# Kernel optimization log

Measured on AMD Instinct MI355X. Metric: run time of the kernel, lower is better.

Reference implementation:

```python
import jax, jax.numpy as jnp
import numpy as np

B, N, C, H = 16, 512, 384, 6
HD = C // H  # 64
FF = 1152


def _ln(x, w, b, eps=1e-5):
    mu = jnp.mean(x, axis=-1, keepdims=True)
    var = jnp.mean((x - mu) ** 2, axis=-1, keepdims=True)
    return (x - mu) * jax.lax.rsqrt(var + eps) * w + b


def setup_inputs() -> dict:
    key = jax.random.key(0)
    ks = jax.random.split(key, 16)
    rn = lambda k, s, sc=0.02: jax.random.normal(k, s, jnp.float32) * sc
    scale = jnp.float32(HD ** -0.5)
    return {
        "src": jax.random.normal(ks[0], (B, N, C), jnp.float32),
        "pre_w": jnp.ones((C,), jnp.float32), "pre_b": jnp.zeros((C,), jnp.float32),
        "qkv_w": rn(ks[1], (3 * C, C)), "qkv_b": jnp.zeros((3 * C,), jnp.float32),
        "scale": scale, "riem_scale": scale, "grassman_scale": scale,
        "conv_w": rn(ks[2], (H, 3 * H), 0.1), "conv_b": jnp.zeros((H,), jnp.float32),
        "proj_w": rn(ks[3], (C, C)), "proj_b": jnp.zeros((C,), jnp.float32),
        "norm1_w": jnp.ones((C,), jnp.float32), "norm1_b": jnp.zeros((C,), jnp.float32),
        "lin1_w": rn(ks[4], (FF, C)), "lin1_b": jnp.zeros((FF,), jnp.float32),
        "lin2_w": rn(ks[5], (C, FF)), "lin2_b": jnp.zeros((C,), jnp.float32),
    }


def reference(src, pre_w, pre_b, qkv_w, qkv_b, scale, riem_scale, grassman_scale,
              conv_w, conv_b, proj_w, proj_b, norm1_w, norm1_b,
              lin1_w, lin1_b, lin2_w, lin2_b):
    x = _ln(src, pre_w, pre_b)
    qkv = (x @ qkv_w.T + qkv_b).reshape(B, N, 3, H, HD)
    qkv = jnp.transpose(qkv, (2, 0, 3, 1, 4))  # [3,B,H,N,HD]
    q, k, v = qkv[0], qkv[1], qkv[2]

    # Grassmann term: orthonormalize tokens-per-head via reduced QR (N>=HD)
    qgr, _ = jnp.linalg.qr(q)  # [B,H,N,HD]
    kgr, _ = jnp.linalg.qr(k)
    dots = jnp.einsum('bhnd,bhmd->bhnm', qgr, kgr)
    # norm over singleton dim then square == elementwise square
    attn_grass = dots ** 2 * grassman_scale

    # Euclidean dot-product term
    qk = jnp.einsum('bhnd,bhmd->bhnm', q, k)
    attn_eucl = qk * scale

    # Riemannian term: pairwise Frobenius norm between rank-1 covariances
    # ||q_i q_i^T - k_j k_j^T||_F = sqrt(||q_i||^4 + ||k_j||^4 - 2 (q_i.k_j)^2)
    qn2 = jnp.sum(q ** 2, axis=-1)  # [B,H,N]
    kn2 = jnp.sum(k ** 2, axis=-1)
    d2 = qn2[..., :, None] ** 2 + kn2[..., None, :] ** 2 - 2.0 * qk ** 2
    attn_riem = jnp.sqrt(jnp.maximum(d2, 0.0)) * riem_scale

    cat = jnp.concatenate([attn_eucl, attn_riem, attn_grass], axis=1)  # [B,3H,N,N]
    mixed = jnp.einsum('bcnm,oc->bonm', cat, conv_w) + conv_b[None, :, None, None]
    attn_ = jax.nn.softmax(mixed, axis=-1)  # [B,H,N,N]

    out = jnp.einsum('bhnm,bhmd->bhnd', attn_, v)
    out = jnp.transpose(out, (0, 2, 1, 3)).reshape(B, N, C)
    out = out @ proj_w.T + proj_b

    src = src + out
    src = _ln(src, norm1_w, norm1_b)
    h = jax.nn.gelu(src @ lin1_w.T + lin1_b, approximate=False)
    src2 = h @ lin2_w.T + lin2_b
    src = src + src2
    return src, attn_
```

## Files before the change

kernel.cpp:

```cpp
#include <hip/hip_runtime.h>
#include <cstdint>
#include <cstddef>

#define DEVI static __device__ __forceinline__

typedef __bf16 bf16x8 __attribute__((ext_vector_type(8)));
typedef float f32x4 __attribute__((ext_vector_type(4)));
typedef unsigned short u16;
typedef unsigned int u32;

DEVI float b2f(u16 h){ u32 x = ((u32)h) << 16; float f; __builtin_memcpy(&f, &x, 4); return f; }
DEVI u16 f2b(float f){ u32 x; __builtin_memcpy(&x, &f, 4); u32 r = (x + 0x7FFFu + ((x >> 16) & 1u)) >> 16; return (u16)r; }

union V16 { uint4 u; bf16x8 v; u16 h[8]; };

DEVI bf16x8 ld16(const u16* p){ V16 t; t.u = *(const uint4*)p; return t.v; }
DEVI f32x4 fzero(){ f32x4 z; z[0]=0.f; z[1]=0.f; z[2]=0.f; z[3]=0.f; return z; }
DEVI f32x4 mm(bf16x8 a, bf16x8 b, f32x4 c){ return __builtin_amdgcn_mfma_f32_16x16x32_bf16(a, b, c, 0, 0, 0); }
DEVI uint4 cvt8(const float* p){
  float4 a = *(const float4*)p, b = *(const float4*)(p + 4);
  V16 t; t.h[0]=f2b(a.x); t.h[1]=f2b(a.y); t.h[2]=f2b(a.z); t.h[3]=f2b(a.w);
  t.h[4]=f2b(b.x); t.h[5]=f2b(b.y); t.h[6]=f2b(b.z); t.h[7]=f2b(b.w); return t.u;
}

__global__ __launch_bounds__(256) void k_ln_src(const float* __restrict__ in, const float* __restrict__ w,
                                                const float* __restrict__ bias, u16* __restrict__ out){
  int wave = threadIdx.x >> 6, lane = threadIdx.x & 63;
  int row = blockIdx.x * 4 + wave;
  const float* p = in + (size_t)row * 384;
  float v[6], s = 0.f, sq = 0.f;
  for(int i = 0; i < 6; i++){ v[i] = p[lane + 64*i]; s += v[i]; sq += v[i]*v[i]; }
  for(int off = 1; off < 64; off <<= 1){ s += __shfl_xor(s, off); sq += __shfl_xor(sq, off); }
  float mu = s * (1.f/384.f), var = sq * (1.f/384.f) - mu*mu;
  float rstd = rsqrtf(fmaxf(var, 0.f) + 1e-5f);
  for(int i = 0; i < 6; i++){
    int j = lane + 64*i;
    out[(size_t)row*384 + j] = f2b((v[i]-mu)*rstd*w[j] + bias[j]);
  }
}

__global__ __launch_bounds__(256) void k_ln_mid(const float* __restrict__ in, const float* __restrict__ w,
                                                const float* __restrict__ bias, u16* __restrict__ outb,
                                                float* __restrict__ outf){
  int wave = threadIdx.x >> 6, lane = threadIdx.x & 63;
  int row = blockIdx.x * 4 + wave;
  const float* p = in + (size_t)row * 384;
  float v[6], s = 0.f, sq = 0.f;
  for(int i = 0; i < 6; i++){ v[i] = p[lane + 64*i]; s += v[i]; sq += v[i]*v[i]; }
  for(int off = 1; off < 64; off <<= 1){ s += __shfl_xor(s, off); sq += __shfl_xor(sq, off); }
  float mu = s * (1.f/384.f), var = sq * (1.f/384.f) - mu*mu;
  float rstd = rsqrtf(fmaxf(var, 0.f) + 1e-5f);
  for(int i = 0; i < 6; i++){
    int j = lane + 64*i;
    float o = (v[i]-mu)*rstd*w[j] + bias[j];
    outb[(size_t)row*384 + j] = f2b(o);
    outf[(size_t)row*384 + j] = o;
  }
}

template<int MODE, int KDIM, int NOUT>
__global__ __launch_bounds__(256,2) void k_gemm(
    const u16* __restrict__ A, const float* __restrict__ W, const float* __restrict__ bias,
    u16* __restrict__ o0, u16* __restrict__ o1, u16* __restrict__ o2,
    const float* __restrict__ res, float* __restrict__ fout)
{
  __shared__ __align__(16) u16 As[128][72];
  __shared__ __align__(16) u16 Bs[128][72];
  const int tid = threadIdx.x, wv = tid >> 6, lane = tid & 63, quad = lane >> 4, l15 = lane & 15;
  constexpr int NB = NOUT / 128;
  const int m0 = (blockIdx.x / NB) * 128, n0 = (blockIdx.x % NB) * 128;
  const int wr = (wv >> 1) * 64, wc = (wv & 1) * 64;
  f32x4 acc[4][4];
  for(int i = 0; i < 4; i++) for(int j = 0; j < 4; j++) acc[i][j] = fzero();
  for(int kt = 0; kt < KDIM; kt += 64){
    for(int i = 0; i < 4; i++){
      int c = tid + i*256; int row = c >> 3, col = (c & 7) * 8;
      *(uint4*)&As[row][col] = *(const uint4*)&A[(size_t)(m0+row)*KDIM + kt + col];
      *(uint4*)&Bs[row][col] = cvt8(&W[(size_t)(n0+row)*KDIM + kt + col]);
    }
    __syncthreads();
    for(int hf = 0; hf < 2; hf++){
      bf16x8 af[4], bf_[4];
      for(int t = 0; t < 4; t++) af[t]  = ld16(&As[wr + t*16 + l15][hf*32 + quad*8]);
      for(int t = 0; t < 4; t++) bf_[t] = ld16(&Bs[wc + t*16 + l15][hf*32 + quad*8]);
      for(int mt = 0; mt < 4; mt++) for(int nt = 0; nt < 4; nt++)
        acc[mt][nt] = mm(af[mt], bf_[nt], acc[mt][nt]);
    }
    __syncthreads();
  }
  for(int mt = 0; mt < 4; mt++) for(int nt = 0; nt < 4; nt++){
    const int gcol = n0 + wc + nt*16 + l15;
    const float bv = bias[gcol];
    for(int r = 0; r < 4; r++){
      const int grow = m0 + wr + mt*16 + quad*4 + r;
      float val = acc[mt][nt][r] + bv;
      if constexpr(MODE == 0){
        int s = gcol / 384, rem = gcol - s*384, h = rem >> 6, d = rem & 63;
        int bb = grow >> 9, n = grow & 511;
        u16* t = (s == 0) ? o0 : ((s == 1) ? o1 : o2);
        t[(((size_t)(bb*6 + h))*512 + n)*64 + d] = f2b(val);
      } else if constexpr(MODE == 1){
        val += res[(size_t)grow*384 + gcol];
        fout[(size_t)grow*384 + gcol] = val;
      } else {
        float g = 0.5f * val * (1.f + erff(val * 0.70710678118654752f));
        o0[(size_t)grow*1152 + gcol] = f2b(g);
      }
    }
  }
}

__global__ __launch_bounds__(256,1) void k_cholqr(
    const u16* __restrict__ qb, const u16* __restrict__ kb,
    u16* __restrict__ aqb, u16* __restrict__ akb,
    float* __restrict__ qn4, float* __restrict__ kn4)
{
  __shared__ float G[64][65];
  __shared__ float invd[64];
  const int tid = threadIdx.x, wv = tid >> 6, lane = tid & 63, quad = lane >> 4, l15 = lane & 15;
  const int blk = blockIdx.x;
  const int isk = blk >= 96; const int bh = isk ? blk - 96 : blk;
  const u16* M = (isk ? kb : qb) + (size_t)bh * 512 * 64;
  u16* Ao = (isk ? akb : aqb) + (size_t)bh * 512 * 64;
  float* n4 = (isk ? kn4 : qn4) + bh * 512;
  for(int rr = tid; rr < 512; rr += 256){
    const u16* p = M + (size_t)rr * 64;
    float s = 0.f;
    for(int i = 0; i < 8; i++){ V16 c; c.u = *(const uint4*)&p[i*8];
      for(int j = 0; j < 8; j++){ float x = b2f(c.h[j]); s += x*x; } }
    n4[rr] = s * s;
  }
  f32x4 g4[4];
  for(int jt = 0; jt < 4; jt++) g4[jt] = fzero();
  for(int k0 = 0; k0 < 512; k0 += 32){
    const u16* base = M + (size_t)(k0 + quad*8) * 64;
    V16 a;
    for(int j = 0; j < 8; j++) a.h[j] = base[(size_t)j*64 + wv*16 + l15];
    for(int jt = 0; jt < 4; jt++){
      V16 bb;
      for(int j = 0; j < 8; j++) bb.h[j] = base[(size_t)j*64 + jt*16 + l15];
      g4[jt] = mm(a.v, bb.v, g4[jt]);
    }
  }
  for(int jt = 0; jt < 4; jt++)
    for(int r = 0; r < 4; r++)
      G[wv*16 + quad*4 + r][jt*16 + l15] = g4[jt][r];
  __syncthreads();
  for(int k = 0; k < 64; k++){
    if(tid == 0){ float pv = sqrtf(fmaxf(G[k][k], 1e-12f)); G[k][k] = pv; invd[k] = 1.f / pv; }
    __syncthreads();
    if(tid > k && tid < 64) G[k][tid] *= invd[k];
    __syncthreads();
    float gkl = G[k][lane];
    for(int i = k + 1 + wv; i < 64; i += 4)
      G[i][lane] -= G[k][i] * gkl;
    __syncthreads();
  }
  for(int rr = tid; rr < 512; rr += 256){
    float m[64];
    const u16* p = M + (size_t)rr * 64;
    for(int i = 0; i < 8; i++){ V16 c; c.u = *(const uint4*)&p[i*8];
      for(int j = 0; j < 8; j++) m[i*8 + j] = b2f(c.h[j]); }
    #pragma unroll
    for(int j = 0; j < 64; j++){
      float yj = m[j] * invd[j];
      m[j] = yj;
      #pragma unroll
      for(int i = j + 1; i < 64; i++) m[i] -= yj * G[j][i];
    }
    for(int i = 0; i < 8; i++){ V16 c;
      for(int j = 0; j < 8; j++) c.h[j] = f2b(m[i*8 + j]);
      *(uint4*)&Ao[(size_t)rr*64 + i*8] = c.u; }
  }
}

__global__ __launch_bounds__(256,2) void k_attn(
    const u16* __restrict__ qb, const u16* __restrict__ kb,
    const u16* __restrict__ aqb, const u16* __restrict__ akb,
    const float* __restrict__ qn4, const float* __restrict__ kn4,
    const float* __restrict__ convw, const float* __restrict__ convb,
    const float* __restrict__ scp, const float* __restrict__ rsp, const float* __restrict__ gsp,
    float* __restrict__ attn)
{
  __shared__ __align__(16) u16 qt[6][16][72];
  __shared__ __align__(16) u16 at[6][16][72];
  __shared__ float cw[108];
  __shared__ float cb[6];
  __shared__ float red[6][16][4];
  const int tid = threadIdx.x, wv = tid >> 6, lane = tid & 63, quad = lane >> 4, l15 = lane & 15;
  const int b = blockIdx.x >> 5, n0 = (blockIdx.x & 31) * 16;
  if(tid < 108) cw[tid] = convw[tid];
  if(tid >= 128 && tid < 134) cb[tid - 128] = convb[tid - 128];
  for(int c = tid; c < 768; c += 256){
    int h = c >> 7, rem = c & 127, row = rem >> 3, col = (rem & 7) * 8;
    size_t off = (((size_t)(b*6 + h)) * 512 + (size_t)(n0 + row)) * 64 + col;
    *(uint4*)&qt[h][row][col] = *(const uint4*)&qb[off];
    *(uint4*)&at[h][row][col] = *(const uint4*)&aqb[off];
  }
  __syncthreads();
  const float sc = scp[0], rs = rsp[0], gs = gsp[0];
  float qn4r[6][4];
  for(int h = 0; h < 6; h++)
    for(int r = 0; r < 4; r++)
      qn4r[h][r] = qn4[(b*6 + h)*512 + n0 + quad*4 + r];
  float S[6][4], recS[6][4];
  for(int o = 0; o < 6; o++) for(int r = 0; r < 4; r++) S[o][r] = 0.f;
  for(int phase = 0; phase < 2; phase++){
    for(int mt = 0; mt < 8; mt++){
      const int mcol = wv*128 + mt*16 + l15;
      float L[6][4];
      for(int o = 0; o < 6; o++){ float c0 = cb[o]; for(int r = 0; r < 4; r++) L[o][r] = c0; }
      #pragma unroll
      for(int h = 0; h < 6; h++){
        const size_t krow = (((size_t)(b*6 + h)) * 512 + mcol) * 64 + quad*8;
        bf16x8 kf0 = ld16(kb + krow),  kf1 = ld16(kb + krow + 32);
        bf16x8 af0 = ld16(akb + krow), af1 = ld16(akb + krow + 32);
        bf16x8 qf0 = ld16(&qt[h][l15][quad*8]), qf1 = ld16(&qt[h][l15][32 + quad*8]);
        bf16x8 gf0 = ld16(&at[h][l15][quad*8]), gf1 = ld16(&at[h][l15][32 + quad*8]);
        f32x4 qk = fzero(); qk = mm(qf0, kf0, qk); qk = mm(qf1, kf1, qk);
        f32x4 dd = fzero(); dd = mm(gf0, af0, dd); dd = mm(gf1, af1, dd);
        float kn = kn4[(b*6 + h)*512 + mcol];
        #pragma unroll
        for(int r = 0; r < 4; r++){
          float q_ = qk[r];
          float e  = q_ * sc;
          float d2 = qn4r[h][r] + kn - 2.f * q_ * q_;
          float ri = rs * sqrtf(fmaxf(d2, 0.f));
          float g  = gs * dd[r] * dd[r];
          #pragma unroll
          for(int o = 0; o < 6; o++)
            L[o][r] += cw[o*18 + h]*e + cw[o*18 + 6 + h]*ri + cw[o*18 + 12 + h]*g;
        }
      }
      if(phase == 0){
        for(int o = 0; o < 6; o++) for(int r = 0; r < 4; r++) S[o][r] += __expf(fminf(L[o][r], 80.f));
      } else {
        for(int o = 0; o < 6; o++) for(int r = 0; r < 4; r++){
          float a = __expf(fminf(L[o][r], 80.f)) * recS[o][r];
          attn[(((size_t)(b*6 + o)) * 512 + (n0 + quad*4 + r)) * 512 + mcol] = a;
        }
      }
    }
    if(phase == 0){
      for(int o = 0; o < 6; o++) for(int r = 0; r < 4; r++){
        float s = S[o][r];
        s += __shfl_xor(s, 1); s += __shfl_xor(s, 2); s += __shfl_xor(s, 4); s += __shfl_xor(s, 8);
        if(l15 == 0) red[o][quad*4 + r][wv] = s;
      }
      __syncthreads();
      for(int o = 0; o < 6; o++) for(int r = 0; r < 4; r++){
        int rw = quad*4 + r;
        recS[o][r] = 1.f / (red[o][rw][0] + red[o][rw][1] + red[o][rw][2] + red[o][rw][3]);
      }
      __syncthreads();
    }
  }
}

__global__ __launch_bounds__(256,2) void k_av(const float* __restrict__ attn, const u16* __restrict__ vb,
                                              u16* __restrict__ av)
{
  __shared__ __align__(16) u16 At[128][72];
  __shared__ __align__(16) u16 Vt[64][72];
  const int tid = threadIdx.x, wv = tid >> 6, lane = tid & 63, quad = lane >> 4, l15 = lane & 15;
  const int blk = blockIdx.x, bh = blk >> 2, n0 = (blk & 3) * 128;
  const int b = bh / 6, h = bh - b * 6;
  const float* Ap = attn + ((size_t)bh * 512 + n0) * 512;
  const u16* Vp = vb + (size_t)bh * 512 * 64;
  f32x4 acc[2][4];
  for(int mt = 0; mt < 2; mt++) for(int nt = 0; nt < 4; nt++) acc[mt][nt] = fzero();
  for(int k0 = 0; k0 < 512; k0 += 64){
    for(int i = 0; i < 4; i++){ int c = tid + i*256; int row = c >> 3, col = (c & 7) * 8;
      *(uint4*)&At[row][col] = cvt8(&Ap[(size_t)row*512 + k0 + col]); }
    for(int i = 0; i < 2; i++){ int c = tid + i*256; int kk = c >> 3, d0 = (c & 7) * 8;
      V16 cu; cu.u = *(const uint4*)&Vp[(size_t)(k0 + kk)*64 + d0];
      for(int j = 0; j < 8; j++) Vt[d0 + j][kk] = cu.h[j]; }
    __syncthreads();
    for(int hf = 0; hf < 2; hf++){
      bf16x8 af[2], bfv[4];
      for(int mt = 0; mt < 2; mt++) af[mt]  = ld16(&At[wv*32 + mt*16 + l15][hf*32 + quad*8]);
      for(int nt = 0; nt < 4; nt++) bfv[nt] = ld16(&Vt[nt*16 + l15][hf*32 + quad*8]);
      for(int mt = 0; mt < 2; mt++) for(int nt = 0; nt < 4; nt++)
        acc[mt][nt] = mm(af[mt], bfv[nt], acc[mt][nt]);
    }
    __syncthreads();
  }
  for(int mt = 0; mt < 2; mt++) for(int nt = 0; nt < 4; nt++) for(int r = 0; r < 4; r++){
    int n = n0 + wv*32 + mt*16 + quad*4 + r, d = nt*16 + l15;
    av[((size_t)(b*512 + n)) * 384 + h*64 + d] = f2b(acc[mt][nt][r]);
  }
}

extern "C" void kernel_launch(void* const* d_in, const int* in_sizes, int n_in,
                              void* d_out, int out_size, void* d_ws, size_t ws_size,
                              hipStream_t stream) {
  (void)in_sizes; (void)n_in; (void)out_size; (void)ws_size;
  const float* src    = (const float*)d_in[0];
  const float* pre_w  = (const float*)d_in[1];
  const float* pre_b  = (const float*)d_in[2];
  const float* qkv_w  = (const float*)d_in[3];
  const float* qkv_b  = (const float*)d_in[4];
  const float* scp    = (const float*)d_in[5];
  const float* rsp    = (const float*)d_in[6];
  const float* gsp    = (const float*)d_in[7];
  const float* convw  = (const float*)d_in[8];
  const float* convb  = (const float*)d_in[9];
  const float* proj_w = (const float*)d_in[10];
  const float* proj_b = (const float*)d_in[11];
  const float* n1w    = (const float*)d_in[12];
  const float* n1b    = (const float*)d_in[13];
  const float* l1w    = (const float*)d_in[14];
  const float* l1b    = (const float*)d_in[15];
  const float* l2w    = (const float*)d_in[16];
  const float* l2b    = (const float*)d_in[17];

  char* ws = (char*)d_ws;
  u16*   xb   = (u16*)(ws + 0);
  u16*   qb   = (u16*)(ws + 6291456);
  u16*   kb_  = (u16*)(ws + 12582912);
  u16*   vb   = (u16*)(ws + 18874368);
  u16*   aqb  = (u16*)(ws + 25165824);
  u16*   akb  = (u16*)(ws + 31457280);
  float* qn4  = (float*)(ws + 37748736);
  float* kn4  = (float*)(ws + 37945344);
  float* y1   = (float*)(ws + 6291456);
  u16*   hb   = (u16*)(ws + 6291456);
  float* x2f  = (float*)(ws + 25165824);
  u16*   attV = xb;
  u16*   x2b  = xb;

  float* out_src  = (float*)d_out;
  float* out_attn = out_src + 3145728;

  k_ln_src<<<2048, 256, 0, stream>>>(src, pre_w, pre_b, xb);
  k_gemm<0, 384, 1152><<<576, 256, 0, stream>>>(xb, qkv_w, qkv_b, qb, kb_, vb, nullptr, nullptr);
  k_cholqr<<<192, 256, 0, stream>>>(qb, kb_, aqb, akb, qn4, kn4);
  k_attn<<<512, 256, 0, stream>>>(qb, kb_, aqb, akb, qn4, kn4, convw, convb, scp, rsp, gsp, out_attn);
  k_av<<<384, 256, 0, stream>>>(out_attn, vb, attV);
  k_gemm<1, 384, 384><<<192, 256, 0, stream>>>(attV, proj_w, proj_b, nullptr, nullptr, nullptr, src, y1);
  k_ln_mid<<<2048, 256, 0, stream>>>(y1, n1w, n1b, x2b, x2f);
  k_gemm<2, 384, 1152><<<576, 256, 0, stream>>>(x2b, l1w, l1b, hb, nullptr, nullptr, nullptr, nullptr);
  k_gemm<1, 1152, 384><<<192, 256, 0, stream>>>(hb, l2w, l2b, nullptr, nullptr, nullptr, x2f, out_src);
}
```

Before: 816.5 us.

## Single-pass attention logits with deferred softmax normalization in AV kernel

The attention kernel no longer computes logits twice (a sum pass and then a write pass). It writes unnormalized exponentials once, saves per-row partial sums split over two column halves, and doubles the grid with a batch-interleaved block mapping. The AV kernel reads the partial sums, normalizes the rows while loading them, and writes the normalized attention back to the output. This removes half of the logit MFMA and transcendental work, but adds an extra read-modify-write of the large attention tensor and reshuffles the workspace buffers.

```diff
diff --git a/kernel.cpp b/kernel.cpp
--- a/kernel.cpp
+++ b/kernel.cpp
@@ -180,7 +180,7 @@
     const float* __restrict__ qn4, const float* __restrict__ kn4,
     const float* __restrict__ convw, const float* __restrict__ convb,
     const float* __restrict__ scp, const float* __restrict__ rsp, const float* __restrict__ gsp,
-    float* __restrict__ attn)
+    float* __restrict__ attn, float* __restrict__ Spart)
 {
   __shared__ __align__(16) u16 qt[6][16][72];
   __shared__ __align__(16) u16 at[6][16][72];
@@ -188,7 +188,10 @@
   __shared__ float cb[6];
   __shared__ float red[6][16][4];
   const int tid = threadIdx.x, wv = tid >> 6, lane = tid & 63, quad = lane >> 4, l15 = lane & 15;
-  const int b = blockIdx.x >> 5, n0 = (blockIdx.x & 31) * 16;
+  const int blk = blockIdx.x;
+  const int b = ((blk & 7) << 1) | ((blk >> 3) & 1);
+  const int r2 = blk >> 4;
+  const int n0 = (r2 & 31) * 16, half = r2 >> 5;
   if(tid < 108) cw[tid] = convw[tid];
   if(tid >= 128 && tid < 134) cb[tid - 128] = convb[tid - 128];
   for(int c = tid; c < 768; c += 256){
@@ -203,75 +206,84 @@
   for(int h = 0; h < 6; h++)
     for(int r = 0; r < 4; r++)
       qn4r[h][r] = qn4[(b*6 + h)*512 + n0 + quad*4 + r];
-  float S[6][4], recS[6][4];
+  float S[6][4];
   for(int o = 0; o < 6; o++) for(int r = 0; r < 4; r++) S[o][r] = 0.f;
-  for(int phase = 0; phase < 2; phase++){
-    for(int mt = 0; mt < 8; mt++){
-      const int mcol = wv*128 + mt*16 + l15;
-      float L[6][4];
-      for(int o = 0; o < 6; o++){ float c0 = cb[o]; for(int r = 0; r < 4; r++) L[o][r] = c0; }
+  for(int mt = 0; mt < 4; mt++){
+    const int mcol = half*256 + wv*64 + mt*16 + l15;
+    float L[6][4];
+    for(int o = 0; o < 6; o++){ float c0 = cb[o]; for(int r = 0; r < 4; r++) L[o][r] = c0; }
+    #pragma unroll
+    for(int h = 0; h < 6; h++){
+      const size_t krow = (((size_t)(b*6 + h)) * 512 + mcol) * 64 + quad*8;
+      bf16x8 kf0 = ld16(kb + krow),  kf1 = ld16(kb + krow + 32);
+      bf16x8 af0 = ld16(akb + krow), af1 = ld16(akb + krow + 32);
+      bf16x8 qf0 = ld16(&qt[h][l15][quad*8]), qf1 = ld16(&qt[h][l15][32 + quad*8]);
+      bf16x8 gf0 = ld16(&at[h][l15][quad*8]), gf1 = ld16(&at[h][l15][32 + quad*8]);
+      f32x4 qk = fzero(); qk = mm(qf0, kf0, qk); qk = mm(qf1, kf1, qk);
+      f32x4 dd = fzero(); dd = mm(gf0, af0, dd); dd = mm(gf1, af1, dd);
+      float kn = kn4[(b*6 + h)*512 + mcol];
       #pragma unroll
-      for(int h = 0; h < 6; h++){
-        const size_t krow = (((size_t)(b*6 + h)) * 512 + mcol) * 64 + quad*8;
-        bf16x8 kf0 = ld16(kb + krow),  kf1 = ld16(kb + krow + 32);
-        bf16x8 af0 = ld16(akb + krow), af1 = ld16(akb + krow + 32);
-        bf16x8 qf0 = ld16(&qt[h][l15][quad*8]), qf1 = ld16(&qt[h][l15][32 + quad*8]);
-        bf16x8 gf0 = ld16(&at[h][l15][quad*8]), gf1 = ld16(&at[h][l15][32 + quad*8]);
-        f32x4 qk = fzero(); qk = mm(qf0, kf0, qk); qk = mm(qf1, kf1, qk);
-        f32x4 dd = fzero(); dd = mm(gf0, af0, dd); dd = mm(gf1, af1, dd);
-        float kn = kn4[(b*6 + h)*512 + mcol];
+      for(int r = 0; r < 4; r++){
+        float q_ = qk[r];
+        float e  = q_ * sc;
+        float d2 = qn4r[h][r] + kn - 2.f * q_ * q_;
+        float ri = rs * sqrtf(fmaxf(d2, 0.f));
+        float g  = gs * dd[r] * dd[r];
         #pragma unroll
-        for(int r = 0; r < 4; r++){
-          float q_ = qk[r];
-          float e  = q_ * sc;
-          float d2 = qn4r[h][r] + kn - 2.f * q_ * q_;
-          float ri = rs * sqrtf(fmaxf(d2, 0.f));
-          float g  = gs * dd[r] * dd[r];
-          #pragma unroll
-          for(int o = 0; o < 6; o++)
-            L[o][r] += cw[o*18 + h]*e + cw[o*18 + 6 + h]*ri + cw[o*18 + 12 + h]*g;
-        }
+        for(int o = 0; o < 6; o++)
+          L[o][r] += cw[o*18 + h]*e + cw[o*18 + 6 + h]*ri + cw[o*18 + 12 + h]*g;
       }
-      if(phase == 0){
-        for(int o = 0; o < 6; o++) for(int r = 0; r < 4; r++) S[o][r] += __expf(fminf(L[o][r], 80.f));
-      } else {
-        for(int o = 0; o < 6; o++) for(int r = 0; r < 4; r++){
-          float a = __expf(fminf(L[o][r], 80.f)) * recS[o][r];
-          attn[(((size_t)(b*6 + o)) * 512 + (n0 + quad*4 + r)) * 512 + mcol] = a;
-        }
-      }
-    }
-    if(phase == 0){
-      for(int o = 0; o < 6; o++) for(int r = 0; r < 4; r++){
-        float s = S[o][r];
-        s += __shfl_xor(s, 1); s += __shfl_xor(s, 2); s += __shfl_xor(s, 4); s += __shfl_xor(s, 8);
-        if(l15 == 0) red[o][quad*4 + r][wv] = s;
-      }
-      __syncthreads();
-      for(int o = 0; o < 6; o++) for(int r = 0; r < 4; r++){
-        int rw = quad*4 + r;
-        recS[o][r] = 1.f / (red[o][rw][0] + red[o][rw][1] + red[o][rw][2] + red[o][rw][3]);
-      }
-      __syncthreads();
-    }
-  }
-}
-
-__global__ __launch_bounds__(256,2) void k_av(const float* __restrict__ attn, const u16* __restrict__ vb,
-                                              u16* __restrict__ av)
+    }
+    for(int o = 0; o < 6; o++) for(int r = 0; r < 4; r++){
+      float e = __expf(fminf(L[o][r], 80.f));
+      S[o][r] += e;
+      attn[(((size_t)(b*6 + o)) * 512 + (n0 + quad*4 + r)) * 512 + mcol] = e;
+    }
+  }
+  for(int o = 0; o < 6; o++) for(int r = 0; r < 4; r++){
+    float s = S[o][r];
+    s += __shfl_xor(s, 1); s += __shfl_xor(s, 2); s += __shfl_xor(s, 4); s += __shfl_xor(s, 8);
+    if(l15 == 0) red[o][quad*4 + r][wv] = s;
+  }
+  __syncthreads();
+  if(tid < 96){
+    int o = tid >> 4, rr = tid & 15;
+    float s = red[o][rr][0] + red[o][rr][1] + red[o][rr][2] + red[o][rr][3];
+    Spart[(((size_t)(b*6 + o)) * 512 + n0 + rr) * 2 + half] = s;
+  }
+}
+
+__global__ __launch_bounds__(256,2) void k_av(float* __restrict__ attn, const u16* __restrict__ vb,
+                                              const float* __restrict__ Spart, u16* __restrict__ av)
 {
   __shared__ __align__(16) u16 At[128][72];
   __shared__ __align__(16) u16 Vt[64][72];
+  __shared__ float recs[128];
   const int tid = threadIdx.x, wv = tid >> 6, lane = tid & 63, quad = lane >> 4, l15 = lane & 15;
   const int blk = blockIdx.x, bh = blk >> 2, n0 = (blk & 3) * 128;
   const int b = bh / 6, h = bh - b * 6;
-  const float* Ap = attn + ((size_t)bh * 512 + n0) * 512;
+  float* Ap = attn + ((size_t)bh * 512 + n0) * 512;
   const u16* Vp = vb + (size_t)bh * 512 * 64;
+  if(tid < 128){
+    size_t si = ((size_t)bh * 512 + n0 + tid) * 2;
+    recs[tid] = 1.f / (Spart[si] + Spart[si + 1]);
+  }
+  __syncthreads();
   f32x4 acc[2][4];
   for(int mt = 0; mt < 2; mt++) for(int nt = 0; nt < 4; nt++) acc[mt][nt] = fzero();
   for(int k0 = 0; k0 < 512; k0 += 64){
-    for(int i = 0; i < 4; i++){ int c = tid + i*256; int row = c >> 3, col = (c & 7) * 8;
-      *(uint4*)&At[row][col] = cvt8(&Ap[(size_t)row*512 + k0 + col]); }
+    for(int i = 0; i < 4; i++){
+      int c = tid + i*256; int row = c >> 3, col = (c & 7) * 8;
+      float* sp = Ap + (size_t)row*512 + k0 + col;
+      float rc = recs[row];
+      float4 x = *(const float4*)sp, y = *(const float4*)(sp + 4);
+      x.x *= rc; x.y *= rc; x.z *= rc; x.w *= rc;
+      y.x *= rc; y.y *= rc; y.z *= rc; y.w *= rc;
+      *(float4*)sp = x; *(float4*)(sp + 4) = y;
+      V16 t; t.h[0]=f2b(x.x); t.h[1]=f2b(x.y); t.h[2]=f2b(x.z); t.h[3]=f2b(x.w);
+      t.h[4]=f2b(y.x); t.h[5]=f2b(y.y); t.h[6]=f2b(y.z); t.h[7]=f2b(y.w);
+      *(uint4*)&At[row][col] = t.u;
+    }
     for(int i = 0; i < 2; i++){ int c = tid + i*256; int kk = c >> 3, d0 = (c & 7) * 8;
       V16 cu; cu.u = *(const uint4*)&Vp[(size_t)(k0 + kk)*64 + d0];
       for(int j = 0; j < 8; j++) Vt[d0 + j][kk] = cu.h[j]; }
@@ -321,13 +333,14 @@
   u16*   vb   = (u16*)(ws + 18874368);
   u16*   aqb  = (u16*)(ws + 25165824);
   u16*   akb  = (u16*)(ws + 31457280);
-  float* qn4  = (float*)(ws + 37748736);
-  float* kn4  = (float*)(ws + 37945344);
+  float* qn4  = (float*)(ws + 0);
+  float* kn4  = (float*)(ws + 196608);
+  float* Spart= (float*)(ws + 393216);
+  u16*   attV = (u16*)(ws + 25165824);
   float* y1   = (float*)(ws + 6291456);
+  u16*   x2b  = (u16*)(ws + 0);
+  float* x2f  = (float*)(ws + 25165824);
   u16*   hb   = (u16*)(ws + 6291456);
-  float* x2f  = (float*)(ws + 25165824);
-  u16*   attV = xb;
-  u16*   x2b  = xb;
 
   float* out_src  = (float*)d_out;
   float* out_attn = out_src + 3145728;
@@ -335,8 +348,8 @@
   k_ln_src<<<2048, 256, 0, stream>>>(src, pre_w, pre_b, xb);
   k_gemm<0, 384, 1152><<<576, 256, 0, stream>>>(xb, qkv_w, qkv_b, qb, kb_, vb, nullptr, nullptr);
   k_cholqr<<<192, 256, 0, stream>>>(qb, kb_, aqb, akb, qn4, kn4);
-  k_attn<<<512, 256, 0, stream>>>(qb, kb_, aqb, akb, qn4, kn4, convw, convb, scp, rsp, gsp, out_attn);
-  k_av<<<384, 256, 0, stream>>>(out_attn, vb, attV);
+  k_attn<<<1024, 256, 0, stream>>>(qb, kb_, aqb, akb, qn4, kn4, convw, convb, scp, rsp, gsp, out_attn, Spart);
+  k_av<<<384, 256, 0, stream>>>(out_attn, vb, Spart, attV);
   k_gemm<1, 384, 384><<<192, 256, 0, stream>>>(attV, proj_w, proj_b, nullptr, nullptr, nullptr, src, y1);
   k_ln_mid<<<2048, 256, 0, stream>>>(y1, n1w, n1b, x2b, x2f);
   k_gemm<2, 384, 1152><<<576, 256, 0, stream>>>(x2b, l1w, l1b, hb, nullptr, nullptr, nullptr, nullptr);
```

After: 666.2 us. 1.23x faster.
